# Kernel tuning notes

Hardware: AMD Instinct MI355X
Metric: run time of the kernel (lower is better)

Reference implementation:

```python
import jax, jax.numpy as jnp
import numpy as np

KNN = 16
BN_EPS = 1e-5


def _swiglu(z, w1, w2, w3):
    # SwiGLU applied over the last dim: w2(silu(w1 z) * (w3 z))
    return (jax.nn.silu(z @ w1.T) * (z @ w3.T)) @ w2.T


def setup_inputs() -> dict:
    key = jax.random.key(0)
    ks = jax.random.split(key, 12)
    B, T, D = 1, 2048, 768
    H, N, KD = 4, 25600, 128
    HID_A, HID_S = 44, 1024
    inp = {
        "x": jax.random.normal(ks[0], (B, T, D), jnp.float32),
        "wq": jax.random.normal(ks[1], (H * KD, D), jnp.float32) * (1.0 / np.sqrt(D)),
        "bq": jax.random.normal(ks[2], (H * KD,), jnp.float32) * 0.02,
        "bn_gamma": jnp.ones((H * KD,), jnp.float32),
        "bn_beta": jnp.zeros((H * KD,), jnp.float32),
        "bn_mean": jnp.zeros((H * KD,), jnp.float32),
        "bn_var": jnp.ones((H * KD,), jnp.float32),
        "keys": jax.random.uniform(ks[3], (H, N, KD), jnp.float32, -1.0 / np.sqrt(KD), 1.0 / np.sqrt(KD)),
        "w_down_tab": jax.random.normal(ks[4], (N, 1), jnp.float32) * 0.02,
        "w_up_tab": jax.random.normal(ks[5], (N, 1), jnp.float32) * 0.02,
        "a_w1": jax.random.normal(ks[6], (HID_A, KNN), jnp.float32) * (1.0 / np.sqrt(KNN)),
        "a_w2": jax.random.normal(ks[7], (KNN, HID_A), jnp.float32) * (1.0 / np.sqrt(HID_A)),
        "a_w3": jax.random.normal(ks[8], (HID_A, KNN), jnp.float32) * (1.0 / np.sqrt(KNN)),
        "s_w1": jax.random.normal(ks[9], (HID_S, D), jnp.float32) * (1.0 / np.sqrt(D)),
        "s_w2": jax.random.normal(ks[10], (D, HID_S), jnp.float32) * (1.0 / np.sqrt(HID_S)),
        "s_w3": jax.random.normal(ks[11], (HID_S, D), jnp.float32) * (1.0 / np.sqrt(D)),
    }
    return inp


def reference(x, wq, bq, bn_gamma, bn_beta, bn_mean, bn_var, keys,
              w_down_tab, w_up_tab, a_w1, a_w2, a_w3, s_w1, s_w2, s_w3):
    B, T, D = x.shape
    H, N, KD = keys.shape
    identity = x
    # query projection + BatchNorm1d (inference: running stats)
    q = x.reshape(-1, D) @ wq.T + bq                      # (bs, H*KD)
    q = (q - bn_mean) * jax.lax.rsqrt(bn_var + BN_EPS) * bn_gamma + bn_beta
    q = q.reshape(-1, H, KD)                              # (bs, H, KD)
    # product-key scoring against full key table, per head
    scores = jnp.einsum('bhk,hnk->bhn', q, keys)          # (bs, H, N)
    top_s, top_i = jax.lax.top_k(scores, KNN)             # (bs, H, KNN)
    gates = jax.nn.softmax(top_s, axis=-1)
    idx = top_i.reshape(B, T, H, KNN)
    gates = gates.reshape(B, T, H, KNN)
    # expert_dim == 1: embedding gather yields a scalar per selected expert
    w_down = w_down_tab[idx, 0]                           # (B, T, H, KNN)
    w_up = w_up_tab[idx, 0]                               # (B, T, H, KNN)
    # einsum('btd,bthkd->bthk') with d-broadcast (expert_dim=1 vs D):
    # equals sum_d x[b,t,d] * w_down[b,t,h,k,0]
    xd = jnp.sum(x, axis=-1)[:, :, None, None] * w_down   # (B, T, H, KNN)
    h = _swiglu(xd, a_w1, a_w2, a_w3)                     # (B, T, H, KNN)
    h = h * gates
    # einsum('bthk,bthkd->btd') with d=1 -> (B, T, 1), broadcasts vs (B,T,D)
    comb = jnp.sum(h * w_up, axis=(2, 3))[:, :, None]     # (B, T, 1)
    out = comb + _swiglu(identity, s_w1, s_w2, s_w3)      # (B, T, D)
    return out
```

## Files before the change

### kernel.cpp

```cpp
#include <hip/hip_runtime.h>
#include <hip/hip_bf16.h>
#include <cmath>

#define NEG_INF (-3.402823466e38f)
#define SPLITS 32
#define SPN    800
#define GRP    32
#define NGRP   25

typedef __attribute__((ext_vector_type(8))) short s16x8;
typedef __attribute__((ext_vector_type(4))) float f32x4;

__device__ __forceinline__ unsigned short f2bf(float f) {
    union { float f; unsigned u; } v; v.f = f;
    unsigned u = v.u;
    u += 0x7fffu + ((u >> 16) & 1u);
    return (unsigned short)(u >> 16);
}

__global__ __launch_bounds__(256) void cvt_all_kernel(
        const float* __restrict__ s0, const float* __restrict__ s1,
        const float* __restrict__ s2, const float* __restrict__ s3,
        const float* __restrict__ s4, const float* __restrict__ keys,
        unsigned short* __restrict__ dst, float* __restrict__ sumx) {
    int i = blockIdx.x * 256 + threadIdx.x;
    if (i >= 4358144) return;
    const float* src; int base;
    if      (i < 393216)  { src = s0;   base = 0; }
    else if (i < 491520)  { src = s1;   base = 393216; }
    else if (i < 688128)  { src = s2;   base = 491520; }
    else if (i < 884736)  { src = s3;   base = 688128; }
    else if (i < 1081344) { src = s4;   base = 884736; }
    else                  { src = keys; base = 1081344; }
    float4 f = ((const float4*)src)[i - base];
    ushort4 o;
    o.x = f2bf(f.x); o.y = f2bf(f.y); o.z = f2bf(f.z); o.w = f2bf(f.w);
    ((ushort4*)dst)[i] = o;
    if (i < 393216) {
        float s = f.x + f.y + f.z + f.w;
        #pragma unroll
        for (int off = 32; off > 0; off >>= 1) s += __shfl_down(s, off);
        if ((threadIdx.x & 63) == 0) atomicAdd(&sumx[i / 192], s);
    }
}

template <int EPI>
__global__ __launch_bounds__(256) void gemm_nt(
        const unsigned short* __restrict__ A, const unsigned short* __restrict__ W,
        int M, int N, int K,
        float* __restrict__ outF, unsigned short* __restrict__ outB,
        const float* __restrict__ p0, const float* __restrict__ p1,
        const float* __restrict__ p2, const float* __restrict__ p3,
        const float* __restrict__ p4) {
    __shared__ alignas(16) short As[64][72];
    __shared__ alignas(16) short Ws[64][72];
    const int tid = threadIdx.x;
    const int m0 = blockIdx.x * 64, n0 = blockIdx.y * 64;
    const int wv = tid >> 6, lane = tid & 63;
    const int wr = wv >> 1, wc = wv & 1;
    const int lr = lane & 15, lq = lane >> 4;
    f32x4 acc[2][2];
    #pragma unroll
    for (int i = 0; i < 2; ++i)
        #pragma unroll
        for (int j = 0; j < 2; ++j) acc[i][j] = (f32x4){0.f, 0.f, 0.f, 0.f};

    for (int kb = 0; kb < K; kb += 64) {
        #pragma unroll
        for (int it = 0; it < 2; ++it) {
            int chunk = tid + it * 256;
            int row = chunk >> 3, c8 = (chunk & 7) * 8;
            *(s16x8*)&As[row][c8] = *(const s16x8*)(A + (size_t)(m0 + row) * K + kb + c8);
            *(s16x8*)&Ws[row][c8] = *(const s16x8*)(W + (size_t)(n0 + row) * K + kb + c8);
        }
        __syncthreads();
        #pragma unroll
        for (int ks = 0; ks < 2; ++ks) {
            const int k0 = ks * 32 + lq * 8;
            #pragma unroll
            for (int rt = 0; rt < 2; ++rt) {
                s16x8 a = *(const s16x8*)&As[wr * 32 + rt * 16 + lr][k0];
                #pragma unroll
                for (int ct = 0; ct < 2; ++ct) {
                    s16x8 b = *(const s16x8*)&Ws[wc * 32 + ct * 16 + lr][k0];
                    acc[rt][ct] = __builtin_amdgcn_mfma_f32_16x16x32_bf16(a, b, acc[rt][ct], 0, 0, 0);
                }
            }
        }
        __syncthreads();
    }
    #pragma unroll
    for (int rt = 0; rt < 2; ++rt)
        #pragma unroll
        for (int ct = 0; ct < 2; ++ct)
            #pragma unroll
            for (int r = 0; r < 4; ++r) {
                int m = m0 + wr * 32 + rt * 16 + lq * 4 + r;
                int n = n0 + wc * 32 + ct * 16 + lr;
                float v = acc[rt][ct][r];
                if (EPI == 0) {
                    float q = v + p0[n];
                    q = (q - p3[n]) * rsqrtf(p4[n] + 1e-5f) * p1[n] + p2[n];
                    outB[(size_t)m * N + n] = f2bf(q);
                } else {
                    outF[(size_t)m * N + n] = v + p0[m];
                }
            }
}

__global__ __launch_bounds__(256) void gemm_swiglu_kernel(
        const unsigned short* __restrict__ A, const unsigned short* __restrict__ W1,
        const unsigned short* __restrict__ W3, int M, int N, int K,
        unsigned short* __restrict__ outB) {
    __shared__ alignas(16) short As[64][72];
    __shared__ alignas(16) short W1s[64][72];
    __shared__ alignas(16) short W3s[64][72];
    const int tid = threadIdx.x;
    const int m0 = blockIdx.x * 64, n0 = blockIdx.y * 64;
    const int wv = tid >> 6, lane = tid & 63;
    const int wr = wv >> 1, wc = wv & 1;
    const int lr = lane & 15, lq = lane >> 4;
    f32x4 acc1[2][2], acc3[2][2];
    #pragma unroll
    for (int i = 0; i < 2; ++i)
        #pragma unroll
        for (int j = 0; j < 2; ++j) {
            acc1[i][j] = (f32x4){0.f, 0.f, 0.f, 0.f};
            acc3[i][j] = (f32x4){0.f, 0.f, 0.f, 0.f};
        }
    for (int kb = 0; kb < K; kb += 64) {
        #pragma unroll
        for (int it = 0; it < 2; ++it) {
            int chunk = tid + it * 256;
            int row = chunk >> 3, c8 = (chunk & 7) * 8;
            *(s16x8*)&As[row][c8]  = *(const s16x8*)(A  + (size_t)(m0 + row) * K + kb + c8);
            *(s16x8*)&W1s[row][c8] = *(const s16x8*)(W1 + (size_t)(n0 + row) * K + kb + c8);
            *(s16x8*)&W3s[row][c8] = *(const s16x8*)(W3 + (size_t)(n0 + row) * K + kb + c8);
        }
        __syncthreads();
        #pragma unroll
        for (int ks = 0; ks < 2; ++ks) {
            const int k0 = ks * 32 + lq * 8;
            #pragma unroll
            for (int rt = 0; rt < 2; ++rt) {
                s16x8 a = *(const s16x8*)&As[wr * 32 + rt * 16 + lr][k0];
                #pragma unroll
                for (int ct = 0; ct < 2; ++ct) {
                    s16x8 b1 = *(const s16x8*)&W1s[wc * 32 + ct * 16 + lr][k0];
                    s16x8 b3 = *(const s16x8*)&W3s[wc * 32 + ct * 16 + lr][k0];
                    acc1[rt][ct] = __builtin_amdgcn_mfma_f32_16x16x32_bf16(a, b1, acc1[rt][ct], 0, 0, 0);
                    acc3[rt][ct] = __builtin_amdgcn_mfma_f32_16x16x32_bf16(a, b3, acc3[rt][ct], 0, 0, 0);
                }
            }
        }
        __syncthreads();
    }
    #pragma unroll
    for (int rt = 0; rt < 2; ++rt)
        #pragma unroll
        for (int ct = 0; ct < 2; ++ct)
            #pragma unroll
            for (int r = 0; r < 4; ++r) {
                int m = m0 + wr * 32 + rt * 16 + lq * 4 + r;
                int n = n0 + wc * 32 + ct * 16 + lr;
                float u1 = acc1[rt][ct][r], u3 = acc3[rt][ct][r];
                float hv = u1 / (1.f + expf(-u1)) * u3;
                outB[(size_t)m * N + n] = f2bf(hv);
            }
}

template <int PASS>
__global__ __launch_bounds__(256, 4) void score_pass_kernel(
        const unsigned short* __restrict__ Q,
        const unsigned short* __restrict__ Kt,
        float* __restrict__ maxbuf,
        const float* __restrict__ theta,
        int* __restrict__ cnt,
        float2* __restrict__ buf) {
    __shared__ alignas(16) short Ks[2][GRP][136];
    const int b = blockIdx.x;
    const int tile = b >> 7;
    const int hsp = b & 127;
    const int h = hsp >> 5, sp = hsp & 31;
    const int w = threadIdx.x >> 6, lane = threadIdx.x & 63;
    const int lr = lane & 15, lq = lane >> 4;
    const int t0 = tile * 256 + w * 64;
    const int nb0 = sp * SPN;

    s16x8 qf[4][4];
    #pragma unroll
    for (int tt = 0; tt < 4; ++tt) {
        const unsigned short* qp = Q + (size_t)(t0 + tt * 16 + lr) * 512 + h * 128 + lq * 8;
        #pragma unroll
        for (int ks = 0; ks < 4; ++ks) qf[tt][ks] = *(const s16x8*)(qp + ks * 32);
    }

    float runmax[4] = {NEG_INF, NEG_INF, NEG_INF, NEG_INF};
    float th[4];
    if (PASS == 2) {
        #pragma unroll
        for (int tt = 0; tt < 4; ++tt) th[tt] = theta[(t0 + tt * 16 + lr) * 4 + h];
    }

    const int srow = threadIdx.x >> 4;
    const int scol = (threadIdx.x & 15) * 8;
    const unsigned short* kgp =
        Kt + ((size_t)h * 25600 + nb0 + srow) * 128 + scol;

    {
        *(s16x8*)&Ks[0][srow][scol]      = *(const s16x8*)kgp;
        *(s16x8*)&Ks[0][srow + 16][scol] = *(const s16x8*)(kgp + 2048);
    }

    for (int g = 0; g < NGRP; ++g) {
        s16x8 ka0, ka1;
        if (g + 1 < NGRP) {
            const unsigned short* kp = kgp + (size_t)(g + 1) * 4096;
            ka0 = *(const s16x8*)kp;
            ka1 = *(const s16x8*)(kp + 2048);
        }
        __syncthreads();
        const int cb = g & 1;
        #pragma unroll
        for (int st = 0; st < 2; ++st) {
            f32x4 acc[4];
            #pragma unroll
            for (int tt = 0; tt < 4; ++tt) acc[tt] = (f32x4){0.f, 0.f, 0.f, 0.f};
            #pragma unroll
            for (int ks = 0; ks < 4; ++ks) {
                s16x8 ka = *(const s16x8*)&Ks[cb][st * 16 + lr][ks * 32 + lq * 8];
                #pragma unroll
                for (int tt = 0; tt < 4; ++tt)
                    acc[tt] = __builtin_amdgcn_mfma_f32_16x16x32_bf16(ka, qf[tt][ks], acc[tt], 0, 0, 0);
            }
            if (PASS == 1) {
                #pragma unroll
                for (int tt = 0; tt < 4; ++tt) {
                    float m0 = fmaxf(fmaxf(acc[tt][0], acc[tt][1]),
                                     fmaxf(acc[tt][2], acc[tt][3]));
                    runmax[tt] = fmaxf(runmax[tt], m0);
                }
            } else {
                const int nb = nb0 + g * GRP + st * 16;
                #pragma unroll
                for (int tt = 0; tt < 4; ++tt) {
                    float m0 = fmaxf(fmaxf(acc[tt][0], acc[tt][1]),
                                     fmaxf(acc[tt][2], acc[tt][3]));
                    if (m0 >= th[tt]) {
                        int g4 = (t0 + tt * 16 + lr) * 4 + h;
                        #pragma unroll
                        for (int r = 0; r < 4; ++r) {
                            if (acc[tt][r] >= th[tt]) {
                                int n = nb + lq * 4 + r;
                                int pos = atomicAdd(&cnt[g4], 1);
                                if (pos < 64) {
                                    float2 e; e.x = acc[tt][r]; e.y = __int_as_float(n);
                                    buf[(size_t)g4 * 64 + pos] = e;
                                }
                            }
                        }
                    }
                }
            }
        }
        if (g + 1 < NGRP) {
            const int nbuf = cb ^ 1;
            *(s16x8*)&Ks[nbuf][srow][scol]      = ka0;
            *(s16x8*)&Ks[nbuf][srow + 16][scol] = ka1;
        }
    }

    if (PASS == 1) {
        #pragma unroll
        for (int tt = 0; tt < 4; ++tt)
            maxbuf[(size_t)((t0 + tt * 16 + lr) * 4 + h) * 128 + sp * 4 + lq] = runmax[tt];
    }
}

__global__ __launch_bounds__(64) void theta_kernel(
        const float* __restrict__ maxbuf, float* __restrict__ theta) {
    int g = blockIdx.x * 64 + threadIdx.x;
    if (g >= 8192) return;
    const float* mb = maxbuf + (size_t)g * 128;
    float s[16];
    #pragma unroll
    for (int i = 0; i < 16; ++i) s[i] = NEG_INF;
    for (int j = 0; j < 128; ++j) {
        float v = mb[j];
        if (v > s[15]) {
            #pragma unroll
            for (int i = 15; i > 0; --i)
                s[i] = (v > s[i - 1]) ? s[i - 1] : ((v > s[i]) ? v : s[i]);
            s[0] = (v > s[0]) ? v : s[0];
        }
    }
    theta[g] = s[15];
}

__global__ __launch_bounds__(256) void finalize_kernel(
        const int* __restrict__ cnt, const float2* __restrict__ buf,
        const float* __restrict__ sumx,
        const float* __restrict__ wdown, const float* __restrict__ wup,
        const float* __restrict__ aw1, const float* __restrict__ aw2,
        const float* __restrict__ aw3, float* __restrict__ combsum) {
    __shared__ float zsh[4][16];
    __shared__ float wsh[4][16];
    const int wv = threadIdx.x >> 6, lane = threadIdx.x & 63;
    const int g = blockIdx.x * 4 + wv;
    const int t = g >> 2;
    int c = cnt[g]; c = (c > 64) ? 64 : c;

    float v = NEG_INF; int n = 0x7fffffff;
    if (lane < c) {
        float2 e = buf[(size_t)g * 64 + lane];
        v = e.x; n = __float_as_int(e.y);
    }
    int r = 0;
    for (int i = 0; i < c; ++i) {
        float vi = __shfl(v, i);
        int   ni = __shfl(n, i);
        r += ((vi > v) || (vi == v && ni < n)) ? 1 : 0;
    }
    float m = v;
    #pragma unroll
    for (int off = 32; off > 0; off >>= 1) m = fmaxf(m, __shfl_xor(m, off));
    const bool sel = (lane < c) && (r < 16);
    float e = sel ? expf(v - m) : 0.f;
    float den = e;
    #pragma unroll
    for (int off = 32; off > 0; off >>= 1) den += __shfl_xor(den, off);
    if (sel) {
        zsh[wv][r] = sumx[t] * wdown[n];
        wsh[wv][r] = (e / den) * wup[n];
    }
    __syncthreads();
    float contrib = 0.f;
    if (lane < 44) {
        float u1 = 0.f, u3 = 0.f, cj = 0.f;
        #pragma unroll
        for (int k = 0; k < 16; ++k) {
            float zk = zsh[wv][k];
            u1 += zk * aw1[lane * 16 + k];
            u3 += zk * aw3[lane * 16 + k];
            cj += wsh[wv][k] * aw2[k * 44 + lane];
        }
        float gj = u1 / (1.f + expf(-u1)) * u3;
        contrib = gj * cj;
    }
    #pragma unroll
    for (int off = 32; off > 0; off >>= 1) contrib += __shfl_xor(contrib, off);
    if (lane == 0) atomicAdd(&combsum[t], contrib);
}

extern "C" void kernel_launch(void* const* d_in, const int* in_sizes, int n_in,
                              void* d_out, int out_size, void* d_ws, size_t ws_size,
                              hipStream_t stream) {
    const float* x     = (const float*)d_in[0];
    const float* wq    = (const float*)d_in[1];
    const float* bq    = (const float*)d_in[2];
    const float* gamma = (const float*)d_in[3];
    const float* beta  = (const float*)d_in[4];
    const float* mean  = (const float*)d_in[5];
    const float* var   = (const float*)d_in[6];
    const float* keys  = (const float*)d_in[7];
    const float* wdown = (const float*)d_in[8];
    const float* wup   = (const float*)d_in[9];
    const float* aw1   = (const float*)d_in[10];
    const float* aw2   = (const float*)d_in[11];
    const float* aw3   = (const float*)d_in[12];
    const float* sw1   = (const float*)d_in[13];
    const float* sw2   = (const float*)d_in[14];
    const float* sw3   = (const float*)d_in[15];
    float* out = (float*)d_out;

    char* ws = (char*)d_ws;
    unsigned short* x_b    = (unsigned short*)(ws + 0);
    unsigned short* wq_b   = (unsigned short*)(ws + 3145728);
    unsigned short* sw1_b  = (unsigned short*)(ws + 3932160);
    unsigned short* sw3_b  = (unsigned short*)(ws + 5505024);
    unsigned short* sw2_b  = (unsigned short*)(ws + 7077888);
    unsigned short* keys_b = (unsigned short*)(ws + 8650752);
    unsigned short* q_b    = (unsigned short*)(ws + 34865152);
    float* sumx    = (float*)(ws + 36962304);
    float* theta   = (float*)(ws + 36970496);
    float* combsum = (float*)(ws + 37003264);
    int*   cnt     = (int*)  (ws + 37011456);
    char* R1 = ws + 37044224;
    float* maxbuf = (float*)R1;
    float2* buf   = (float2*)R1;
    unsigned short* h_b = (unsigned short*)R1;

    hipMemsetAsync(ws + 36962304, 0, 81920, stream);
    cvt_all_kernel<<<17024, 256, 0, stream>>>(x, wq, sw1, sw3, sw2, keys, x_b, sumx);

    gemm_nt<0><<<dim3(32, 8), 256, 0, stream>>>(x_b, wq_b, 2048, 512, 768,
                                                nullptr, q_b, bq, gamma, beta, mean, var);
    score_pass_kernel<1><<<1024, 256, 0, stream>>>(q_b, keys_b, maxbuf, nullptr, nullptr, nullptr);
    theta_kernel<<<128, 64, 0, stream>>>(maxbuf, theta);
    score_pass_kernel<2><<<1024, 256, 0, stream>>>(q_b, keys_b, nullptr, theta, cnt, buf);
    finalize_kernel<<<2048, 256, 0, stream>>>(cnt, buf, sumx, wdown, wup, aw1, aw2, aw3, combsum);
    gemm_swiglu_kernel<<<dim3(32, 16), 256, 0, stream>>>(x_b, sw1_b, sw3_b, 2048, 1024, 768, h_b);
    gemm_nt<2><<<dim3(32, 12), 256, 0, stream>>>(h_b, sw2_b, 2048, 768, 1024,
                                                 out, nullptr, combsum,
                                                 nullptr, nullptr, nullptr, nullptr);
}
```

Before: 353.1 us.

## Co-schedule shared-expert SwiGLU GEMMs with score passes in fused mega-kernels

Merges the shared SwiGLU up-projection GEMM with score pass 1, and the down-projection GEMM with score pass 2, into two heterogeneous kernels that dispatch on block index. The aim is to fill the GPU with independent work and overlap compute-bound GEMM tiles with the score passes. Finalize now adds the combined MoE term directly into the output row instead of using atomics and a bias epilogue, which removes the separate combsum step. The fused path needs a larger workspace (it checks ws_size and falls back otherwise). The larger shared-memory footprint of the score blocks may reduce occupancy.

New measurement: 313.9 us. 11.1% less time.

```diff
diff --git a/kernel.cpp b/kernel.cpp
--- a/kernel.cpp
+++ b/kernel.cpp
@@ -108,15 +108,14 @@
             }
 }
 
-__global__ __launch_bounds__(256) void gemm_swiglu_kernel(
-        const unsigned short* __restrict__ A, const unsigned short* __restrict__ W1,
-        const unsigned short* __restrict__ W3, int M, int N, int K,
-        unsigned short* __restrict__ outB) {
-    __shared__ alignas(16) short As[64][72];
-    __shared__ alignas(16) short W1s[64][72];
-    __shared__ alignas(16) short W3s[64][72];
-    const int tid = threadIdx.x;
-    const int m0 = blockIdx.x * 64, n0 = blockIdx.y * 64;
+__device__ __forceinline__ void swiglu_body(
+        int sb, int tid, const unsigned short* __restrict__ A,
+        const unsigned short* __restrict__ W1, const unsigned short* __restrict__ W3,
+        unsigned short* __restrict__ outB, char* smem) {
+    short (*As)[72]  = (short(*)[72])smem;
+    short (*W1s)[72] = (short(*)[72])(smem + 9216);
+    short (*W3s)[72] = (short(*)[72])(smem + 18432);
+    const int m0 = (sb & 31) * 64, n0 = (sb >> 5) * 64;
     const int wv = tid >> 6, lane = tid & 63;
     const int wr = wv >> 1, wc = wv & 1;
     const int lr = lane & 15, lq = lane >> 4;
@@ -128,14 +127,14 @@
             acc1[i][j] = (f32x4){0.f, 0.f, 0.f, 0.f};
             acc3[i][j] = (f32x4){0.f, 0.f, 0.f, 0.f};
         }
-    for (int kb = 0; kb < K; kb += 64) {
+    for (int kb = 0; kb < 768; kb += 64) {
         #pragma unroll
         for (int it = 0; it < 2; ++it) {
             int chunk = tid + it * 256;
             int row = chunk >> 3, c8 = (chunk & 7) * 8;
-            *(s16x8*)&As[row][c8]  = *(const s16x8*)(A  + (size_t)(m0 + row) * K + kb + c8);
-            *(s16x8*)&W1s[row][c8] = *(const s16x8*)(W1 + (size_t)(n0 + row) * K + kb + c8);
-            *(s16x8*)&W3s[row][c8] = *(const s16x8*)(W3 + (size_t)(n0 + row) * K + kb + c8);
+            *(s16x8*)&As[row][c8]  = *(const s16x8*)(A  + (size_t)(m0 + row) * 768 + kb + c8);
+            *(s16x8*)&W1s[row][c8] = *(const s16x8*)(W1 + (size_t)(n0 + row) * 768 + kb + c8);
+            *(s16x8*)&W3s[row][c8] = *(const s16x8*)(W3 + (size_t)(n0 + row) * 768 + kb + c8);
         }
         __syncthreads();
         #pragma unroll
@@ -165,24 +164,72 @@
                 int n = n0 + wc * 32 + ct * 16 + lr;
                 float u1 = acc1[rt][ct][r], u3 = acc3[rt][ct][r];
                 float hv = u1 / (1.f + expf(-u1)) * u3;
-                outB[(size_t)m * N + n] = f2bf(hv);
+                outB[(size_t)m * 1024 + n] = f2bf(hv);
+            }
+}
+
+__device__ __forceinline__ void down_body(
+        int sb, int tid, const unsigned short* __restrict__ A,
+        const unsigned short* __restrict__ W, float* __restrict__ outF,
+        char* smem) {
+    short (*As)[72] = (short(*)[72])smem;
+    short (*Ws)[72] = (short(*)[72])(smem + 9216);
+    const int m0 = (sb & 31) * 64, n0 = (sb >> 5) * 64;
+    const int wv = tid >> 6, lane = tid & 63;
+    const int wr = wv >> 1, wc = wv & 1;
+    const int lr = lane & 15, lq = lane >> 4;
+    f32x4 acc[2][2];
+    #pragma unroll
+    for (int i = 0; i < 2; ++i)
+        #pragma unroll
+        for (int j = 0; j < 2; ++j) acc[i][j] = (f32x4){0.f, 0.f, 0.f, 0.f};
+    for (int kb = 0; kb < 1024; kb += 64) {
+        #pragma unroll
+        for (int it = 0; it < 2; ++it) {
+            int chunk = tid + it * 256;
+            int row = chunk >> 3, c8 = (chunk & 7) * 8;
+            *(s16x8*)&As[row][c8] = *(const s16x8*)(A + (size_t)(m0 + row) * 1024 + kb + c8);
+            *(s16x8*)&Ws[row][c8] = *(const s16x8*)(W + (size_t)(n0 + row) * 1024 + kb + c8);
+        }
+        __syncthreads();
+        #pragma unroll
+        for (int ks = 0; ks < 2; ++ks) {
+            const int k0 = ks * 32 + lq * 8;
+            #pragma unroll
+            for (int rt = 0; rt < 2; ++rt) {
+                s16x8 a = *(const s16x8*)&As[wr * 32 + rt * 16 + lr][k0];
+                #pragma unroll
+                for (int ct = 0; ct < 2; ++ct) {
+                    s16x8 b = *(const s16x8*)&Ws[wc * 32 + ct * 16 + lr][k0];
+                    acc[rt][ct] = __builtin_amdgcn_mfma_f32_16x16x32_bf16(a, b, acc[rt][ct], 0, 0, 0);
+                }
+            }
+        }
+        __syncthreads();
+    }
+    #pragma unroll
+    for (int rt = 0; rt < 2; ++rt)
+        #pragma unroll
+        for (int ct = 0; ct < 2; ++ct)
+            #pragma unroll
+            for (int r = 0; r < 4; ++r) {
+                int m = m0 + wr * 32 + rt * 16 + lq * 4 + r;
+                int n = n0 + wc * 32 + ct * 16 + lr;
+                outF[(size_t)m * 768 + n] = acc[rt][ct][r];
             }
 }
 
 template <int PASS>
-__global__ __launch_bounds__(256, 4) void score_pass_kernel(
-        const unsigned short* __restrict__ Q,
-        const unsigned short* __restrict__ Kt,
-        float* __restrict__ maxbuf,
-        const float* __restrict__ theta,
-        int* __restrict__ cnt,
-        float2* __restrict__ buf) {
-    __shared__ alignas(16) short Ks[2][GRP][136];
-    const int b = blockIdx.x;
+__device__ __forceinline__ void score_body(
+        int b, int tid,
+        const unsigned short* __restrict__ Q, const unsigned short* __restrict__ Kt,
+        float* __restrict__ maxbuf, const float* __restrict__ theta,
+        int* __restrict__ cnt, float2* __restrict__ buf, char* smem) {
+    short (*Ks)[GRP][136] = (short(*)[GRP][136])smem;
     const int tile = b >> 7;
     const int hsp = b & 127;
     const int h = hsp >> 5, sp = hsp & 31;
-    const int w = threadIdx.x >> 6, lane = threadIdx.x & 63;
+    const int w = tid >> 6, lane = tid & 63;
     const int lr = lane & 15, lq = lane >> 4;
     const int t0 = tile * 256 + w * 64;
     const int nb0 = sp * SPN;
@@ -202,8 +249,8 @@
         for (int tt = 0; tt < 4; ++tt) th[tt] = theta[(t0 + tt * 16 + lr) * 4 + h];
     }
 
-    const int srow = threadIdx.x >> 4;
-    const int scol = (threadIdx.x & 15) * 8;
+    const int srow = tid >> 4;
+    const int scol = (tid & 15) * 8;
     const unsigned short* kgp =
         Kt + ((size_t)h * 25600 + nb0 + srow) * 128 + scol;
 
@@ -277,6 +324,42 @@
     }
 }
 
+template <int PASS>
+__global__ __launch_bounds__(256, 4) void score_pass_kernel(
+        const unsigned short* __restrict__ Q, const unsigned short* __restrict__ Kt,
+        float* __restrict__ maxbuf, const float* __restrict__ theta,
+        int* __restrict__ cnt, float2* __restrict__ buf) {
+    __shared__ alignas(16) char smem[17408];
+    score_body<PASS>(blockIdx.x, threadIdx.x, Q, Kt, maxbuf, theta, cnt, buf, smem);
+}
+
+__global__ __launch_bounds__(256, 4) void megaA_kernel(
+        const unsigned short* __restrict__ xb, const unsigned short* __restrict__ w1,
+        const unsigned short* __restrict__ w3, unsigned short* __restrict__ hb,
+        const unsigned short* __restrict__ Q, const unsigned short* __restrict__ Kt,
+        float* __restrict__ maxbuf) {
+    __shared__ alignas(16) char smem[27648];
+    if (blockIdx.x < 512)
+        swiglu_body(blockIdx.x, threadIdx.x, xb, w1, w3, hb, smem);
+    else
+        score_body<1>(blockIdx.x - 512, threadIdx.x, Q, Kt, maxbuf,
+                      nullptr, nullptr, nullptr, smem);
+}
+
+__global__ __launch_bounds__(256, 4) void megaB_kernel(
+        const unsigned short* __restrict__ hb, const unsigned short* __restrict__ w2,
+        float* __restrict__ outF,
+        const unsigned short* __restrict__ Q, const unsigned short* __restrict__ Kt,
+        const float* __restrict__ theta, int* __restrict__ cnt,
+        float2* __restrict__ buf) {
+    __shared__ alignas(16) char smem[18432];
+    if (blockIdx.x < 384)
+        down_body(blockIdx.x, threadIdx.x, hb, w2, outF, smem);
+    else
+        score_body<2>(blockIdx.x - 384, threadIdx.x, Q, Kt, nullptr,
+                      theta, cnt, buf, smem);
+}
+
 __global__ __launch_bounds__(64) void theta_kernel(
         const float* __restrict__ maxbuf, float* __restrict__ theta) {
     int g = blockIdx.x * 64 + threadIdx.x;
@@ -297,17 +380,20 @@
     theta[g] = s[15];
 }
 
+template <int FUSE_OUT>
 __global__ __launch_bounds__(256) void finalize_kernel(
         const int* __restrict__ cnt, const float2* __restrict__ buf,
         const float* __restrict__ sumx,
         const float* __restrict__ wdown, const float* __restrict__ wup,
         const float* __restrict__ aw1, const float* __restrict__ aw2,
-        const float* __restrict__ aw3, float* __restrict__ combsum) {
+        const float* __restrict__ aw3, float* __restrict__ combsum,
+        float* __restrict__ out) {
     __shared__ float zsh[4][16];
     __shared__ float wsh[4][16];
+    __shared__ float csh[4];
     const int wv = threadIdx.x >> 6, lane = threadIdx.x & 63;
-    const int g = blockIdx.x * 4 + wv;
-    const int t = g >> 2;
+    const int t = blockIdx.x;
+    const int g = t * 4 + wv;
     int c = cnt[g]; c = (c > 64) ? 64 : c;
 
     float v = NEG_INF; int n = 0x7fffffff;
@@ -349,7 +435,23 @@
     }
     #pragma unroll
     for (int off = 32; off > 0; off >>= 1) contrib += __shfl_xor(contrib, off);
-    if (lane == 0) atomicAdd(&combsum[t], contrib);
+    if (FUSE_OUT) {
+        if (lane == 0) csh[wv] = contrib;
+        __syncthreads();
+        float comb = csh[0] + csh[1] + csh[2] + csh[3];
+        float* orow = out + (size_t)t * 768;
+        #pragma unroll
+        for (int i = 0; i < 3; ++i) orow[threadIdx.x + i * 256] += comb;
+    } else {
+        if (lane == 0) atomicAdd(&combsum[t], contrib);
+    }
+}
+
+__global__ __launch_bounds__(256) void gemm_swiglu_kernel(
+        const unsigned short* __restrict__ A, const unsigned short* __restrict__ W1,
+        const unsigned short* __restrict__ W3, unsigned short* __restrict__ outB) {
+    __shared__ alignas(16) char smem[27648];
+    swiglu_body(blockIdx.x, threadIdx.x, A, W1, W3, outB, smem);
 }
 
 extern "C" void kernel_launch(void* const* d_in, const int* in_sizes, int n_in,
@@ -388,19 +490,31 @@
     char* R1 = ws + 37044224;
     float* maxbuf = (float*)R1;
     float2* buf   = (float2*)R1;
-    unsigned short* h_b = (unsigned short*)R1;
+    unsigned short* h_b_fused = (unsigned short*)(ws + 41238528);
+    const bool fused = ws_size >= 45432832ull;
 
     hipMemsetAsync(ws + 36962304, 0, 81920, stream);
     cvt_all_kernel<<<17024, 256, 0, stream>>>(x, wq, sw1, sw3, sw2, keys, x_b, sumx);
-
     gemm_nt<0><<<dim3(32, 8), 256, 0, stream>>>(x_b, wq_b, 2048, 512, 768,
                                                 nullptr, q_b, bq, gamma, beta, mean, var);
-    score_pass_kernel<1><<<1024, 256, 0, stream>>>(q_b, keys_b, maxbuf, nullptr, nullptr, nullptr);
-    theta_kernel<<<128, 64, 0, stream>>>(maxbuf, theta);
-    score_pass_kernel<2><<<1024, 256, 0, stream>>>(q_b, keys_b, nullptr, theta, cnt, buf);
-    finalize_kernel<<<2048, 256, 0, stream>>>(cnt, buf, sumx, wdown, wup, aw1, aw2, aw3, combsum);
-    gemm_swiglu_kernel<<<dim3(32, 16), 256, 0, stream>>>(x_b, sw1_b, sw3_b, 2048, 1024, 768, h_b);
-    gemm_nt<2><<<dim3(32, 12), 256, 0, stream>>>(h_b, sw2_b, 2048, 768, 1024,
-                                                 out, nullptr, combsum,
-                                                 nullptr, nullptr, nullptr, nullptr);
-}
+    if (fused) {
+        megaA_kernel<<<1536, 256, 0, stream>>>(x_b, sw1_b, sw3_b, h_b_fused,
+                                               q_b, keys_b, maxbuf);
+        theta_kernel<<<128, 64, 0, stream>>>(maxbuf, theta);
+        megaB_kernel<<<1408, 256, 0, stream>>>(h_b_fused, sw2_b, out,
+                                               q_b, keys_b, theta, cnt, buf);
+        finalize_kernel<1><<<2048, 256, 0, stream>>>(cnt, buf, sumx, wdown, wup,
+                                                     aw1, aw2, aw3, combsum, out);
+    } else {
+        unsigned short* h_b = (unsigned short*)R1;
+        score_pass_kernel<1><<<1024, 256, 0, stream>>>(q_b, keys_b, maxbuf, nullptr, nullptr, nullptr);
+        theta_kernel<<<128, 64, 0, stream>>>(maxbuf, theta);
+        score_pass_kernel<2><<<1024, 256, 0, stream>>>(q_b, keys_b, nullptr, theta, cnt, buf);
+        finalize_kernel<0><<<2048, 256, 0, stream>>>(cnt, buf, sumx, wdown, wup,
+                                                     aw1, aw2, aw3, combsum, nullptr);
+        gemm_swiglu_kernel<<<512, 256, 0, stream>>>(x_b, sw1_b, sw3_b, h_b);
+        gemm_nt<2><<<dim3(32, 12), 256, 0, stream>>>(h_b, sw2_b, 2048, 768, 1024,
+                                                     out, nullptr, combsum,
+                                                     nullptr, nullptr, nullptr, nullptr);
+    }
+}
```
